# Kernel tuning notes

Hardware: AMD Instinct MI355X
Metric: run time of the kernel (lower is better)

Reference implementation:

```python
import jax, jax.numpy as jnp
import numpy as np

IN_F = 4096
OUT_F = 4096
GROUP = 128  # group_size divides in_features, so groups are contiguous along in dim


def setup_inputs() -> dict:
    key = jax.random.key(0)
    k1, k2, k3 = jax.random.split(key, 3)
    x = jax.random.normal(k1, (4, 2048, IN_F), dtype=jnp.float32)
    # ternary codes in {-1, 0, +1}
    ternary = (jax.random.randint(k2, (OUT_F, IN_F), 0, 3) - 1).astype(jnp.int8)
    n_groups = OUT_F * IN_F // GROUP
    # per-group positive scales (abs-mean init in the original)
    scales = jax.random.uniform(k3, (n_groups,), dtype=jnp.float32, minval=0.01, maxval=0.1)
    return {"x": x, "ternary": ternary, "scales": scales}


def reference(x, ternary, scales):
    # Dequantize: scales are per contiguous group of GROUP weights in the
    # flattened (out*in) layout; since IN_F % GROUP == 0 this is
    # [OUT_F, IN_F//GROUP] groups along the in dimension.
    s = scales.reshape(OUT_F, IN_F // GROUP, 1)                 # [O, G, 1]
    w = (ternary.astype(jnp.float32).reshape(OUT_F, IN_F // GROUP, GROUP) * s)
    w = w.reshape(OUT_F, IN_F)                                   # dense float weight
    # y = x @ W^T  (F.linear with no bias)
    return jnp.einsum("bsi,oi->bso", x, w)
```

## Files before the change

### kernel.cpp

```cpp
#include <hip/hip_runtime.h>


#define IN_F  4096
#define OUT_F 4096
#define MROWS 8192
#define GROUP 128

#define BM 256
#define BN 256
#define BK 64
#define NKT   (IN_F / BK)
#define NITER (NKT / 2)

#define PREP_BLOCKS 2048

using bf16x8 = __attribute__((ext_vector_type(8))) __bf16;
using f32x16 = __attribute__((ext_vector_type(16))) float;

#define GLOBAL_AS __attribute__((address_space(1)))
#define LDS_AS    __attribute__((address_space(3)))

__device__ __forceinline__ unsigned short f2bf(float f) {
  unsigned int u = __float_as_uint(f);
  u += 0x7fffu + ((u >> 16) & 1u);
  return (unsigned short)(u >> 16);
}

__global__ void prep_kernel(const float* __restrict__ x, unsigned short* __restrict__ xb,
                            const int* __restrict__ t, const float* __restrict__ s,
                            unsigned short* __restrict__ wb) {
  const int stride = PREP_BLOCKS * 256;
  const int gid = blockIdx.x * 256 + threadIdx.x;
  for (int i = gid; i < (MROWS * IN_F) / 8; i += stride) {
    const int e = i * 8;
    const float4 a0 = *(const float4*)(x + e);
    const float4 a1 = *(const float4*)(x + e + 4);
    union { unsigned short u[8]; uint4 v; } o;
    o.u[0] = f2bf(a0.x); o.u[1] = f2bf(a0.y); o.u[2] = f2bf(a0.z); o.u[3] = f2bf(a0.w);
    o.u[4] = f2bf(a1.x); o.u[5] = f2bf(a1.y); o.u[6] = f2bf(a1.z); o.u[7] = f2bf(a1.w);
    *(uint4*)(xb + e) = o.v;
  }
  for (int i = gid; i < (OUT_F * IN_F) / 8; i += stride) {
    const int e = i * 8;
    const float sc = s[e >> 7];
    const int4 t0 = *(const int4*)(t + e);
    const int4 t1 = *(const int4*)(t + e + 4);
    union { unsigned short u[8]; uint4 v; } o;
    o.u[0] = f2bf((float)t0.x * sc); o.u[1] = f2bf((float)t0.y * sc);
    o.u[2] = f2bf((float)t0.z * sc); o.u[3] = f2bf((float)t0.w * sc);
    o.u[4] = f2bf((float)t1.x * sc); o.u[5] = f2bf((float)t1.y * sc);
    o.u[6] = f2bf((float)t1.z * sc); o.u[7] = f2bf((float)t1.w * sc);
    *(uint4*)(wb + e) = o.v;
  }
}


#define FENCE asm volatile("" ::: "memory")
#define BAR() do { FENCE; __builtin_amdgcn_s_barrier(); FENCE; } while (0)
#define VMBAR(N) do { asm volatile("s_waitcnt vmcnt(" #N ")" ::: "memory"); \
                      __builtin_amdgcn_s_barrier(); FENCE; } while (0)

__global__ __launch_bounds__(512, 2) void gemm_bt_kernel(const unsigned short* __restrict__ A,
                                                         const unsigned short* __restrict__ B,
                                                         float* __restrict__ C) {
  __shared__ unsigned short lds[65536];

  const int tid  = threadIdx.x;
  const int lane = tid & 63;
  const int wv   = tid >> 6;
  const int wm   = wv & 1;
  const int wn   = wv >> 1;
  const int r32  = lane & 31;
  const int kh   = lane >> 5;

  const int bid = blockIdx.x;
  const int xcd = bid & 7;
  const int loc = bid >> 3;
  const int by  = (xcd >> 1) * 8 + (loc >> 3);
  const int bx  = (xcd & 1) * 8 + (loc & 7);
  const int m0  = by * BM;
  const int n0  = bx * BN;

  const int srow = lane >> 3;
  const int l7   = lane & 7;
  const int rowoff0 = (wv * 2 + 0) * 8 + srow;
  const int rowoff1 = (wv * 2 + 1) * 8 + srow;
  const int sc0 = (l7 ^ srow ^ ((wv * 2 + 0) & 7)) * 8;
  const int sc1 = (l7 ^ srow ^ ((wv * 2 + 1) & 7)) * 8;
  const unsigned short* pA0 = A + (size_t)(m0 + rowoff0) * IN_F + sc0;
  const unsigned short* pA1 = A + (size_t)(m0 + rowoff1) * IN_F + sc1;
  const unsigned short* pB0 = B + (size_t)(n0 + rowoff0) * IN_F + sc0;
  const unsigned short* pB1 = B + (size_t)(n0 + rowoff1) * IN_F + sc1;

#define STAGE_A(bufi, h, kcol) do { \
    __builtin_amdgcn_global_load_lds((const GLOBAL_AS unsigned int*)(pA0 + (size_t)(h) * 128 * IN_F + (kcol)), \
        (LDS_AS unsigned int*)((char*)lds + (bufi) * 32768 + (h) * 16384 + (wv * 2 + 0) * 1024), 16, 0, 0); \
    __builtin_amdgcn_global_load_lds((const GLOBAL_AS unsigned int*)(pA1 + (size_t)(h) * 128 * IN_F + (kcol)), \
        (LDS_AS unsigned int*)((char*)lds + (bufi) * 32768 + (h) * 16384 + (wv * 2 + 1) * 1024), 16, 0, 0); \
  } while (0)

#define STAGE_B(bufi, h, kcol) do { \
    __builtin_amdgcn_global_load_lds((const GLOBAL_AS unsigned int*)(pB0 + (size_t)(h) * 128 * IN_F + (kcol)), \
        (LDS_AS unsigned int*)((char*)lds + 65536 + (bufi) * 32768 + (h) * 16384 + (wv * 2 + 0) * 1024), 16, 0, 0); \
    __builtin_amdgcn_global_load_lds((const GLOBAL_AS unsigned int*)(pB1 + (size_t)(h) * 128 * IN_F + (kcol)), \
        (LDS_AS unsigned int*)((char*)lds + 65536 + (bufi) * 32768 + (h) * 16384 + (wv * 2 + 1) * 1024), 16, 0, 0); \
  } while (0)

  const int rA = wm * 64 + r32;
  const int rB = wn * 32 + r32;
  int offA[2][4];
  int offB[4];
#pragma unroll
  for (int sm = 0; sm < 2; ++sm) {
    const int fh = ((sm * 4) + (r32 >> 3)) & 7;
#pragma unroll
    for (int k4 = 0; k4 < 4; ++k4) {
      const int pc = (2 * k4 + kh) ^ (r32 & 7) ^ fh;
      offA[sm][k4] = (rA + sm * 32) * 128 + pc * 16;
    }
  }
  {
    const int fh = ((wn * 4) + (r32 >> 3)) & 7;
#pragma unroll
    for (int k4 = 0; k4 < 4; ++k4) {
      const int pc = (2 * k4 + kh) ^ (r32 & 7) ^ fh;
      offB[k4] = 65536 + rB * 128 + pc * 16;
    }
  }

  bf16x8 af[2][4], bf[2][4];

#define READ_A(bufi, qm) do { \
    _Pragma("unroll") for (int sm = 0; sm < 2; ++sm) \
    _Pragma("unroll") for (int k4 = 0; k4 < 4; ++k4) \
      af[sm][k4] = *(const bf16x8*)((const char*)lds + offA[sm][k4] + (bufi) * 32768 + (qm) * 16384); \
  } while (0)

#define READ_B(bufi, qn) do { \
    _Pragma("unroll") for (int k4 = 0; k4 < 4; ++k4) \
      bf[qn][k4] = *(const bf16x8*)((const char*)lds + offB[k4] + (bufi) * 32768 + (qn) * 16384); \
  } while (0)

#define MFMA_Q(qm, qn) do { \
    __builtin_amdgcn_s_setprio(1); \
    _Pragma("unroll") for (int sm = 0; sm < 2; ++sm) \
    _Pragma("unroll") for (int k4 = 0; k4 < 4; ++k4) \
      acc[qm][sm][qn] = __builtin_amdgcn_mfma_f32_32x32x16_bf16(af[sm][k4], bf[qn][k4], acc[qm][sm][qn], 0, 0, 0); \
    __builtin_amdgcn_s_setprio(0); \
  } while (0)

  f32x16 acc[2][2][2];
#pragma unroll
  for (int a = 0; a < 2; ++a)
#pragma unroll
    for (int b = 0; b < 2; ++b)
#pragma unroll
      for (int c = 0; c < 2; ++c)
        acc[a][b][c] = (f32x16)(0.0f);

  STAGE_A(0, 0, 0); STAGE_B(0, 0, 0); STAGE_B(0, 1, 0); STAGE_A(0, 1, 0);
  STAGE_A(1, 0, BK); STAGE_B(1, 0, BK); STAGE_B(1, 1, BK);
  VMBAR(6);

#pragma unroll 1
  for (int j = 0; j < NITER; ++j) {
    const int ku = (2 * j + 1) * BK;
    const int k2 = (2 * j + 2) * BK;
    const int k3 = (2 * j + 3) * BK;
    const bool more = (j < NITER - 1);

    READ_A(0, 0); READ_B(0, 0);
    STAGE_A(1, 1, ku);
    BAR(); MFMA_Q(0, 0); BAR();

    READ_B(0, 1);
    if (more) STAGE_A(0, 0, k2);
    BAR(); MFMA_Q(0, 1); BAR();

    READ_A(0, 1);
    if (more) STAGE_B(0, 0, k2);
    BAR(); MFMA_Q(1, 0); BAR();

    if (more) STAGE_B(0, 1, k2);
    BAR(); MFMA_Q(1, 1);
    if (more) { VMBAR(6); } else { VMBAR(0); }

    READ_A(1, 0); READ_B(1, 0);
    if (more) STAGE_A(0, 1, k2);
    BAR(); MFMA_Q(0, 0); BAR();

    READ_B(1, 1);
    if (more) STAGE_A(1, 0, k3);
    BAR(); MFMA_Q(0, 1); BAR();

    READ_A(1, 1);
    if (more) STAGE_B(1, 0, k3);
    BAR(); MFMA_Q(1, 0); BAR();

    if (more) STAGE_B(1, 1, k3);
    BAR(); MFMA_Q(1, 1);
    if (more) { VMBAR(6); } else { BAR(); }
  }

#pragma unroll
  for (int qm = 0; qm < 2; ++qm)
#pragma unroll
    for (int sm = 0; sm < 2; ++sm)
#pragma unroll
      for (int qn = 0; qn < 2; ++qn) {
        const int ncol = n0 + qn * 128 + wn * 32 + r32;
        const int mb   = m0 + qm * 128 + wm * 64 + sm * 32 + 4 * kh;
#pragma unroll
        for (int r = 0; r < 16; ++r) {
          const int mrow = mb + (r & 3) + 8 * (r >> 2);
          C[(size_t)mrow * OUT_F + ncol] = acc[qm][sm][qn][r];
        }
      }
}

extern "C" void kernel_launch(void* const* d_in, const int* in_sizes, int n_in,
                              void* d_out, int out_size, void* d_ws, size_t ws_size,
                              hipStream_t stream) {
  const float* x       = (const float*)d_in[0];
  const int*   ternary = (const int*)d_in[1];
  const float* scales  = (const float*)d_in[2];
  float* out = (float*)d_out;

  unsigned short* xb = (unsigned short*)d_ws;
  unsigned short* wb = xb + (size_t)MROWS * IN_F;

  prep_kernel<<<PREP_BLOCKS, 256, 0, stream>>>(x, xb, ternary, scales, wb);

  gemm_bt_kernel<<<(MROWS / BM) * (OUT_F / BN), 512, 0, stream>>>(xb, wb, out);
}
```

Measured before the change: 525.5 us.

## Fuse bf16 conversion and ternary dequant into GEMM tile loads

Removes the separate prep kernel that converted x to bf16 and dequantized the ternary weights into a workspace. The GEMM now loads fp32 activations and int32 ternary codes plus scales into registers, converts and scales them, and writes bf16 into LDS with a register-staged double buffer and one barrier per K tile. This drops the workspace round trip and a kernel launch. In exchange, every tile re-reads fp32 and int32 data (twice the bytes of bf16) from global memory across many blocks, and it gives up async global-to-LDS loads for register staging with more VGPR pressure.

```diff
diff --git a/kernel.cpp b/kernel.cpp
--- a/kernel.cpp
+++ b/kernel.cpp
@@ -4,65 +4,29 @@
 #define IN_F  4096
 #define OUT_F 4096
 #define MROWS 8192
-#define GROUP 128
 
 #define BM 256
 #define BN 256
 #define BK 64
-#define NKT   (IN_F / BK)
-#define NITER (NKT / 2)
-
-#define PREP_BLOCKS 2048
+#define NKT (IN_F / BK)
 
 using bf16x8 = __attribute__((ext_vector_type(8))) __bf16;
 using f32x16 = __attribute__((ext_vector_type(16))) float;
 
-#define GLOBAL_AS __attribute__((address_space(1)))
-#define LDS_AS    __attribute__((address_space(3)))
-
-__device__ __forceinline__ unsigned short f2bf(float f) {
-  unsigned int u = __float_as_uint(f);
-  u += 0x7fffu + ((u >> 16) & 1u);
-  return (unsigned short)(u >> 16);
-}
-
-__global__ void prep_kernel(const float* __restrict__ x, unsigned short* __restrict__ xb,
-                            const int* __restrict__ t, const float* __restrict__ s,
-                            unsigned short* __restrict__ wb) {
-  const int stride = PREP_BLOCKS * 256;
-  const int gid = blockIdx.x * 256 + threadIdx.x;
-  for (int i = gid; i < (MROWS * IN_F) / 8; i += stride) {
-    const int e = i * 8;
-    const float4 a0 = *(const float4*)(x + e);
-    const float4 a1 = *(const float4*)(x + e + 4);
-    union { unsigned short u[8]; uint4 v; } o;
-    o.u[0] = f2bf(a0.x); o.u[1] = f2bf(a0.y); o.u[2] = f2bf(a0.z); o.u[3] = f2bf(a0.w);
-    o.u[4] = f2bf(a1.x); o.u[5] = f2bf(a1.y); o.u[6] = f2bf(a1.z); o.u[7] = f2bf(a1.w);
-    *(uint4*)(xb + e) = o.v;
-  }
-  for (int i = gid; i < (OUT_F * IN_F) / 8; i += stride) {
-    const int e = i * 8;
-    const float sc = s[e >> 7];
-    const int4 t0 = *(const int4*)(t + e);
-    const int4 t1 = *(const int4*)(t + e + 4);
-    union { unsigned short u[8]; uint4 v; } o;
-    o.u[0] = f2bf((float)t0.x * sc); o.u[1] = f2bf((float)t0.y * sc);
-    o.u[2] = f2bf((float)t0.z * sc); o.u[3] = f2bf((float)t0.w * sc);
-    o.u[4] = f2bf((float)t1.x * sc); o.u[5] = f2bf((float)t1.y * sc);
-    o.u[6] = f2bf((float)t1.z * sc); o.u[7] = f2bf((float)t1.w * sc);
-    *(uint4*)(wb + e) = o.v;
-  }
-}
+#define FENCE asm volatile("" ::: "memory")
+#define TILEBAR() do { \
+    asm volatile("s_waitcnt lgkmcnt(0)" ::: "memory"); \
+    __builtin_amdgcn_sched_barrier(0); \
+    __builtin_amdgcn_s_barrier(); \
+    __builtin_amdgcn_sched_barrier(0); \
+    FENCE; \
+  } while (0)
 
 
-#define FENCE asm volatile("" ::: "memory")
-#define BAR() do { FENCE; __builtin_amdgcn_s_barrier(); FENCE; } while (0)
-#define VMBAR(N) do { asm volatile("s_waitcnt vmcnt(" #N ")" ::: "memory"); \
-                      __builtin_amdgcn_s_barrier(); FENCE; } while (0)
-
-__global__ __launch_bounds__(512, 2) void gemm_bt_kernel(const unsigned short* __restrict__ A,
-                                                         const unsigned short* __restrict__ B,
-                                                         float* __restrict__ C) {
+__global__ __launch_bounds__(512, 2) void fused_gemm(const float* __restrict__ X,
+                                                     const int* __restrict__ T,
+                                                     const float* __restrict__ S,
+                                                     float* __restrict__ C) {
   __shared__ unsigned short lds[65536];
 
   const int tid  = threadIdx.x;
@@ -72,6 +36,8 @@
   const int wn   = wv >> 1;
   const int r32  = lane & 31;
   const int kh   = lane >> 5;
+  const int srow = lane >> 3;
+  const int l7   = lane & 7;
 
   const int bid = blockIdx.x;
   const int xcd = bid & 7;
@@ -81,33 +47,53 @@
   const int m0  = by * BM;
   const int n0  = bx * BN;
 
-  const int srow = lane >> 3;
-  const int l7   = lane & 7;
-  const int rowoff0 = (wv * 2 + 0) * 8 + srow;
-  const int rowoff1 = (wv * 2 + 1) * 8 + srow;
-  const int sc0 = (l7 ^ srow ^ ((wv * 2 + 0) & 7)) * 8;
-  const int sc1 = (l7 ^ srow ^ ((wv * 2 + 1) & 7)) * 8;
-  const unsigned short* pA0 = A + (size_t)(m0 + rowoff0) * IN_F + sc0;
-  const unsigned short* pA1 = A + (size_t)(m0 + rowoff1) * IN_F + sc1;
-  const unsigned short* pB0 = B + (size_t)(n0 + rowoff0) * IN_F + sc0;
-  const unsigned short* pB1 = B + (size_t)(n0 + rowoff1) * IN_F + sc1;
+  int offGA[4], offGB[4], sgB[4], ldsA[4], ldsB[4];
+#pragma unroll
+  for (int hi = 0; hi < 4; ++hi) {
+    const int h  = hi >> 1, i = hi & 1;
+    const int ch = wv * 2 + i;
+    const int row = h * 128 + ch * 8 + srow;
+    const int gc  = l7 ^ srow ^ (ch & 7);
+    offGA[hi] = (m0 + row) * IN_F + gc * 8;
+    offGB[hi] = (n0 + row) * IN_F + gc * 8;
+    sgB[hi]   = (n0 + row) * (IN_F / 128);
+    ldsA[hi]  = h * 16384 + ch * 1024 + lane * 16;
+    ldsB[hi]  = 65536 + h * 16384 + ch * 1024 + lane * 16;
+  }
 
-#define STAGE_A(bufi, h, kcol) do { \
-    __builtin_amdgcn_global_load_lds((const GLOBAL_AS unsigned int*)(pA0 + (size_t)(h) * 128 * IN_F + (kcol)), \
-        (LDS_AS unsigned int*)((char*)lds + (bufi) * 32768 + (h) * 16384 + (wv * 2 + 0) * 1024), 16, 0, 0); \
-    __builtin_amdgcn_global_load_lds((const GLOBAL_AS unsigned int*)(pA1 + (size_t)(h) * 128 * IN_F + (kcol)), \
-        (LDS_AS unsigned int*)((char*)lds + (bufi) * 32768 + (h) * 16384 + (wv * 2 + 1) * 1024), 16, 0, 0); \
+  float4 rA[8];
+  int4   rB[8];
+  float  rS[4];
+
+#define ISSUE_T(kt) do { const int kc_ = (kt) * BK; \
+    _Pragma("unroll") for (int hi = 0; hi < 4; ++hi) { \
+      rA[hi*2+0] = *(const float4*)(X + offGA[hi] + kc_); \
+      rA[hi*2+1] = *(const float4*)(X + offGA[hi] + kc_ + 4); } \
+    _Pragma("unroll") for (int hi = 0; hi < 4; ++hi) { \
+      rB[hi*2+0] = *(const int4*)(T + offGB[hi] + kc_); \
+      rB[hi*2+1] = *(const int4*)(T + offGB[hi] + kc_ + 4); \
+      rS[hi] = S[sgB[hi] + ((kc_) >> 7)]; } \
   } while (0)
 
-#define STAGE_B(bufi, h, kcol) do { \
-    __builtin_amdgcn_global_load_lds((const GLOBAL_AS unsigned int*)(pB0 + (size_t)(h) * 128 * IN_F + (kcol)), \
-        (LDS_AS unsigned int*)((char*)lds + 65536 + (bufi) * 32768 + (h) * 16384 + (wv * 2 + 0) * 1024), 16, 0, 0); \
-    __builtin_amdgcn_global_load_lds((const GLOBAL_AS unsigned int*)(pB1 + (size_t)(h) * 128 * IN_F + (kcol)), \
-        (LDS_AS unsigned int*)((char*)lds + 65536 + (bufi) * 32768 + (h) * 16384 + (wv * 2 + 1) * 1024), 16, 0, 0); \
+#define CVTWRITE(cd) do { \
+    _Pragma("unroll") for (int hi = 0; hi < 4; ++hi) { \
+      bf16x8 oa; \
+      oa[0] = (__bf16)rA[hi*2+0].x; oa[1] = (__bf16)rA[hi*2+0].y; \
+      oa[2] = (__bf16)rA[hi*2+0].z; oa[3] = (__bf16)rA[hi*2+0].w; \
+      oa[4] = (__bf16)rA[hi*2+1].x; oa[5] = (__bf16)rA[hi*2+1].y; \
+      oa[6] = (__bf16)rA[hi*2+1].z; oa[7] = (__bf16)rA[hi*2+1].w; \
+      *(bf16x8*)((char*)lds + (cd) * 32768 + ldsA[hi]) = oa; } \
+    _Pragma("unroll") for (int hi = 0; hi < 4; ++hi) { \
+      const float s0_ = rS[hi]; bf16x8 ob; \
+      ob[0] = (__bf16)((float)rB[hi*2+0].x * s0_); ob[1] = (__bf16)((float)rB[hi*2+0].y * s0_); \
+      ob[2] = (__bf16)((float)rB[hi*2+0].z * s0_); ob[3] = (__bf16)((float)rB[hi*2+0].w * s0_); \
+      ob[4] = (__bf16)((float)rB[hi*2+1].x * s0_); ob[5] = (__bf16)((float)rB[hi*2+1].y * s0_); \
+      ob[6] = (__bf16)((float)rB[hi*2+1].z * s0_); ob[7] = (__bf16)((float)rB[hi*2+1].w * s0_); \
+      *(bf16x8*)((char*)lds + (cd) * 32768 + ldsB[hi]) = ob; } \
   } while (0)
 
-  const int rA = wm * 64 + r32;
-  const int rB = wn * 32 + r32;
+  const int rA_ = wm * 64 + r32;
+  const int rB_ = wn * 32 + r32;
   int offA[2][4];
   int offB[4];
 #pragma unroll
@@ -116,7 +102,7 @@
 #pragma unroll
     for (int k4 = 0; k4 < 4; ++k4) {
       const int pc = (2 * k4 + kh) ^ (r32 & 7) ^ fh;
-      offA[sm][k4] = (rA + sm * 32) * 128 + pc * 16;
+      offA[sm][k4] = (rA_ + sm * 32) * 128 + pc * 16;
     }
   }
   {
@@ -124,21 +110,21 @@
 #pragma unroll
     for (int k4 = 0; k4 < 4; ++k4) {
       const int pc = (2 * k4 + kh) ^ (r32 & 7) ^ fh;
-      offB[k4] = 65536 + rB * 128 + pc * 16;
+      offB[k4] = 65536 + rB_ * 128 + pc * 16;
     }
   }
 
   bf16x8 af[2][4], bf[2][4];
 
-#define READ_A(bufi, qm) do { \
+#define READ_A(cb, qm) do { \
     _Pragma("unroll") for (int sm = 0; sm < 2; ++sm) \
     _Pragma("unroll") for (int k4 = 0; k4 < 4; ++k4) \
-      af[sm][k4] = *(const bf16x8*)((const char*)lds + offA[sm][k4] + (bufi) * 32768 + (qm) * 16384); \
+      af[sm][k4] = *(const bf16x8*)((const char*)lds + offA[sm][k4] + (cb) * 32768 + (qm) * 16384); \
   } while (0)
 
-#define READ_B(bufi, qn) do { \
+#define READ_B(cb, qn) do { \
     _Pragma("unroll") for (int k4 = 0; k4 < 4; ++k4) \
-      bf[qn][k4] = *(const bf16x8*)((const char*)lds + offB[k4] + (bufi) * 32768 + (qn) * 16384); \
+      bf[qn][k4] = *(const bf16x8*)((const char*)lds + offB[k4] + (cb) * 32768 + (qn) * 16384); \
   } while (0)
 
 #define MFMA_Q(qm, qn) do { \
@@ -155,51 +141,30 @@
 #pragma unroll
     for (int b = 0; b < 2; ++b)
 #pragma unroll
-      for (int c = 0; c < 2; ++c)
-        acc[a][b][c] = (f32x16)(0.0f);
+      for (int c2 = 0; c2 < 2; ++c2)
+        acc[a][b][c2] = (f32x16)(0.0f);
 
-  STAGE_A(0, 0, 0); STAGE_B(0, 0, 0); STAGE_B(0, 1, 0); STAGE_A(0, 1, 0);
-  STAGE_A(1, 0, BK); STAGE_B(1, 0, BK); STAGE_B(1, 1, BK);
-  VMBAR(6);
+  ISSUE_T(0);
+  CVTWRITE(0);
+  ISSUE_T(1);
+  TILEBAR();
 
+  int c = 0;
 #pragma unroll 1
-  for (int j = 0; j < NITER; ++j) {
-    const int ku = (2 * j + 1) * BK;
-    const int k2 = (2 * j + 2) * BK;
-    const int k3 = (2 * j + 3) * BK;
-    const bool more = (j < NITER - 1);
+  for (int t = 0; t < NKT; ++t) {
+    if (t + 1 < NKT) CVTWRITE(c ^ 1);
+    if (t + 2 < NKT) ISSUE_T(t + 2);
 
-    READ_A(0, 0); READ_B(0, 0);
-    STAGE_A(1, 1, ku);
-    BAR(); MFMA_Q(0, 0); BAR();
+    READ_A(c, 0); READ_B(c, 0);
+    MFMA_Q(0, 0);
+    READ_B(c, 1);
+    MFMA_Q(0, 1);
+    READ_A(c, 1);
+    MFMA_Q(1, 0);
+    MFMA_Q(1, 1);
 
-    READ_B(0, 1);
-    if (more) STAGE_A(0, 0, k2);
-    BAR(); MFMA_Q(0, 1); BAR();
-
-    READ_A(0, 1);
-    if (more) STAGE_B(0, 0, k2);
-    BAR(); MFMA_Q(1, 0); BAR();
-
-    if (more) STAGE_B(0, 1, k2);
-    BAR(); MFMA_Q(1, 1);
-    if (more) { VMBAR(6); } else { VMBAR(0); }
-
-    READ_A(1, 0); READ_B(1, 0);
-    if (more) STAGE_A(0, 1, k2);
-    BAR(); MFMA_Q(0, 0); BAR();
-
-    READ_B(1, 1);
-    if (more) STAGE_A(1, 0, k3);
-    BAR(); MFMA_Q(0, 1); BAR();
-
-    READ_A(1, 1);
-    if (more) STAGE_B(1, 0, k3);
-    BAR(); MFMA_Q(1, 0); BAR();
-
-    if (more) STAGE_B(1, 1, k3);
-    BAR(); MFMA_Q(1, 1);
-    if (more) { VMBAR(6); } else { BAR(); }
+    TILEBAR();
+    c ^= 1;
   }
 
 #pragma unroll
@@ -226,10 +191,7 @@
   const float* scales  = (const float*)d_in[2];
   float* out = (float*)d_out;
 
-  unsigned short* xb = (unsigned short*)d_ws;
-  unsigned short* wb = xb + (size_t)MROWS * IN_F;
+  (void)d_ws; (void)ws_size;
 
-  prep_kernel<<<PREP_BLOCKS, 256, 0, stream>>>(x, xb, ternary, scales, wb);
-
-  gemm_bt_kernel<<<(MROWS / BM) * (OUT_F / BN), 512, 0, stream>>>(xb, wb, out);
+  fused_gemm<<<(MROWS / BM) * (OUT_F / BN), 512, 0, stream>>>(x, ternary, scales, out);
 }
```

Result: slower. 1.711 ms (+225.6%).
